# Optimization experiments

Measured on AMD Instinct MI355X. Metric: run time of the kernel, lower is better.

## Reference

```python
import jax, jax.numpy as jnp
import numpy as np

H_TOK = 57
W_TOK = 57
OUT_HW = 800
NUM_MASKS = 64  # static upper bound on sam mask ids per image


def setup_inputs() -> dict:
    key = jax.random.key(0)
    k = jax.random.split(key, 6)
    B, C, C8, L = 2, 768, 96, 21
    return {
        "embeddings": jax.random.normal(k[0], (B, H_TOK * W_TOK, C), dtype=jnp.float32),
        "sam_masks_label": jax.random.randint(k[1], (B, OUT_HW, OUT_HW), 0, NUM_MASKS, dtype=jnp.int32),
        "conv1_w": jax.random.normal(k[2], (C8, C), dtype=jnp.float32) * 0.02,
        "conv1_b": jax.random.normal(k[3], (C8,), dtype=jnp.float32) * 0.02,
        "conv2_w": jax.random.normal(k[4], (L, C8), dtype=jnp.float32) * 0.02,
        "conv2_b": jax.random.normal(k[5], (L,), dtype=jnp.float32) * 0.02,
    }


def _segment_mean_add(xb, lb):
    # xb: [H, W, C8] features; lb: [H, W] int mask ids.
    C8 = xb.shape[-1]
    seg = lb.reshape(-1)                      # [HW]
    xf = xb.reshape(-1, C8)                   # [HW, C8]
    sums = jax.ops.segment_sum(xf, seg, num_segments=NUM_MASKS)          # [M, C8]
    cnt = jax.ops.segment_sum(jnp.ones_like(seg, dtype=xf.dtype), seg, num_segments=NUM_MASKS)  # [M]
    means = sums / jnp.maximum(cnt, 1.0)[:, None]                        # empty segments -> 0, skipped
    return (xf + means[seg]).reshape(xb.shape)


def reference(embeddings, sam_masks_label, conv1_w, conv1_b, conv2_w, conv2_b):
    C = conv1_w.shape[1]
    e = embeddings.reshape(-1, H_TOK, W_TOK, C)            # [B, 57, 57, C] (NHWC)
    # conv1 (1x1) + relu, channels-last
    x = jax.nn.relu(jnp.einsum("bhwc,oc->bhwo", e, conv1_w) + conv1_b)
    # bilinear resize to 800x800, align_corners=False (half-pixel) == jax 'linear'
    B, _, _, C8 = x.shape
    x = jax.image.resize(x, (B, OUT_HW, OUT_HW, C8), method="linear")
    # per-mask segment mean added back (segments are disjoint so order-free)
    x = jax.vmap(_segment_mean_add)(x, sam_masks_label)
    # conv2 (1x1), return NCHW like torch
    out = jnp.einsum("bhwc,oc->bohw", x, conv2_w) + conv2_b[None, :, None, None]
    return out
```

## Files before the change

kernel.cpp:

```cpp
#include <hip/hip_runtime.h>

#define H_TOKN 57
#define OUT_HW 800
#define NMASK 64
#define C_IN 768
#define C8N 96
#define L_OUT 21
#define NPIX 3249
#define M_TOT 6498
#define YSTR 24
#define SCALE (57.0f/800.0f)

#define BM 32
#define ESTR 40
#define HSTR 97

#define TILE_H 25
#define TILE_W 100
#define ROWS_T 4
#define COLS_T 10
#define NTAPS 40
#define YTSTR 28
#define IPAD 264
#define ZPAD 264
#define ZROWS 32
#define NSLICE 256
#define PSTR 28

#define RCSTR 28
#define MFSTR 28
#define FROWS 8

static __device__ __forceinline__ unsigned short f2bf(float f) {
  unsigned u = __float_as_uint(f);
  u += 0x7FFFu + ((u >> 16) & 1u);
  return (unsigned short)(u >> 16);
}

using bf16x8 = __attribute__((ext_vector_type(8))) short;
using f32x4  = __attribute__((ext_vector_type(4))) float;

static __device__ __forceinline__ ushort4 cvt4(float4 v) {
  ushort4 s; s.x = f2bf(v.x); s.y = f2bf(v.y); s.z = f2bf(v.z); s.w = f2bf(v.w);
  return s;
}

__global__ __launch_bounds__(256) void fused_conv_kernel(
    const float* __restrict__ e, const float* __restrict__ w1,
    const float* __restrict__ b1, const float* __restrict__ w2,
    float* __restrict__ y57)
{
  __shared__ __align__(16) unsigned short eA[2][BM * ESTR];
  __shared__ __align__(16) unsigned short wB[2][C8N * ESTR];
  __shared__ __align__(16) float h_lds[BM * HSTR];
  __shared__ float w2_lds[L_OUT * C8N];
  __shared__ float b1_lds[C8N];

  const int tid = threadIdx.x;
  const int m0 = blockIdx.x * BM;
  const int lane = tid & 63;
  const int wv = tid >> 6;
  const int l15 = lane & 15;
  const int khi = (lane >> 4) << 3;
  const int wm = wv & 1;
  const int wn = wv >> 1;

  for (int i = tid; i < L_OUT * C8N; i += 256) w2_lds[i] = w2[i];
  if (tid < C8N) b1_lds[tid] = b1[tid];

  const int er = tid >> 3, ec4 = (tid & 7) << 2;
  int ep = m0 + er; if (ep >= M_TOT) ep = M_TOT - 1;
  const float* eptr = e + (size_t)ep * C_IN + ec4;
  const float* wptr[3];
  int wr_[3], wc4_[3];
  #pragma unroll
  for (int q = 0; q < 3; ++q) {
    int f = tid + q * 256;
    wr_[q] = f >> 3; wc4_[q] = (f & 7) << 2;
    wptr[q] = w1 + (size_t)wr_[q] * C_IN + wc4_[q];
  }

  f32x4 acc[3];
  #pragma unroll
  for (int t = 0; t < 3; ++t) acc[t] = (f32x4){0.f, 0.f, 0.f, 0.f};

  float4 eReg = *(const float4*)(eptr);
  float4 wReg0 = *(const float4*)(wptr[0]);
  float4 wReg1 = *(const float4*)(wptr[1]);
  float4 wReg2 = *(const float4*)(wptr[2]);

  int cur = 0;
  for (int k0 = 0; k0 < C_IN; k0 += 32, cur ^= 1) {
    *(ushort4*)&eA[cur][er * ESTR + ec4] = cvt4(eReg);
    *(ushort4*)&wB[cur][wr_[0] * ESTR + wc4_[0]] = cvt4(wReg0);
    *(ushort4*)&wB[cur][wr_[1] * ESTR + wc4_[1]] = cvt4(wReg1);
    *(ushort4*)&wB[cur][wr_[2] * ESTR + wc4_[2]] = cvt4(wReg2);
    if (k0 + 32 < C_IN) {
      eReg  = *(const float4*)(eptr + k0 + 32);
      wReg0 = *(const float4*)(wptr[0] + k0 + 32);
      wReg1 = *(const float4*)(wptr[1] + k0 + 32);
      wReg2 = *(const float4*)(wptr[2] + k0 + 32);
    }
    __syncthreads();
    bf16x8 a = *(bf16x8*)&eA[cur][(wm * 16 + l15) * ESTR + khi];
    #pragma unroll
    for (int tt = 0; tt < 3; ++tt) {
      bf16x8 b = *(bf16x8*)&wB[cur][((wn * 3 + tt) * 16 + l15) * ESTR + khi];
      acc[tt] = __builtin_amdgcn_mfma_f32_16x16x32_bf16(a, b, acc[tt], 0, 0, 0);
    }
  }
  __syncthreads();
  #pragma unroll
  for (int tt = 0; tt < 3; ++tt) {
    int n = (wn * 3 + tt) * 16 + l15;
    float bv = b1_lds[n];
    #pragma unroll
    for (int r = 0; r < 4; ++r) {
      int pl = wm * 16 + ((lane >> 4) << 2) + r;
      h_lds[pl * HSTR + n] = fmaxf(acc[tt][r] + bv, 0.f);
    }
  }
  __syncthreads();
  for (int i = tid; i < BM * 24; i += 256) {
    int px = i & (BM - 1), l = i >> 5;
    float s = 0.f;
    if (l < L_OUT) {
      const float* hr = &h_lds[px * HSTR];
      const float* wr = &w2_lds[l * C8N];
      #pragma unroll 8
      for (int c = 0; c < C8N; ++c) s += hr[c] * wr[c];
    }
    int pp = m0 + px;
    if (pp < M_TOT) y57[(size_t)pp * YSTR + l] = s;
  }
}

__global__ __launch_bounds__(256) void binsum_kernel(
    const int* __restrict__ labels, const float* __restrict__ y57,
    float* __restrict__ part)
{
  __shared__ __align__(16) unsigned short It[NMASK * IPAD];
  __shared__ __align__(16) unsigned short zT[ZROWS * ZPAD];
  __shared__ __align__(16) float ytile[NTAPS * YTSTR];
  const int tid = threadIdx.x;
  const int lane = tid & 63, wv = tid >> 6;
  const int l15 = lane & 15, khi = (lane >> 4) << 3;
  const int wc0 = blockIdx.x * TILE_W;
  const int hr0 = blockIdx.y * TILE_H;
  const int b = blockIdx.z;

  for (int i = tid; i < NMASK * IPAD / 2; i += 256) ((unsigned*)It)[i] = 0u;
  for (int i = tid; i < ZROWS * ZPAD / 2; i += 256) ((unsigned*)zT)[i] = 0u;

  float thb = fminf(fmaxf((hr0 + 0.5f) * SCALE - 0.5f, 0.f), 56.f);
  const int ib = min((int)thb, 55);
  float twb = fminf(fmaxf((wc0 + 0.5f) * SCALE - 0.5f, 0.f), 56.f);
  const int jb = min((int)twb, 55);

  const float* yb = y57 + (size_t)b * NPIX * YSTR;
  for (int i = tid; i < NTAPS * 6; i += 256) {
    int t = i / 6, q = (i - t * 6) * 4;
    int r = t / COLS_T, cc = t - r * COLS_T;
    int I = min(ib + r, 56), J = min(jb + cc, 56);
    *(float4*)&ytile[t * YTSTR + q] =
        *(const float4*)(yb + ((size_t)I * H_TOKN + J) * YSTR + q);
  }

  const bool valid = tid < 250;
  const int dh = tid / 10;
  const int dwb = (tid - dh * 10) * 10;
  const int hh = hr0 + dh;
  float th = fminf(fmaxf((hh + 0.5f) * SCALE - 0.5f, 0.f), 56.f);
  int i0 = min((int)th, 55);
  const float fh = th - (float)i0;
  const int ri = i0 - ib;
  const int* lrow = labels + ((size_t)b * OUT_HW + hh) * OUT_HW;

  f32x4 acc0 = {0.f,0.f,0.f,0.f}, acc1 = {0.f,0.f,0.f,0.f};
  int prevm = 0;
  const unsigned short one = 0x3F80;

  float u0[24], u1[24];
  int curj = -1000;
  #define LOADU(U, rj) { \
    const float* ta = &ytile[(ri * COLS_T + (rj)) * YTSTR]; \
    const float* tc = ta + COLS_T * YTSTR; \
    _Pragma("unroll") \
    for (int q = 0; q < 6; ++q) { \
      float4 A = *(const float4*)(ta + 4 * q); \
      float4 C = *(const float4*)(tc + 4 * q); \
      U[4*q+0] = A.x + fh * (C.x - A.x); \
      U[4*q+1] = A.y + fh * (C.y - A.y); \
      U[4*q+2] = A.z + fh * (C.z - A.z); \
      U[4*q+3] = A.w + fh * (C.w - A.w); } }

  __syncthreads();
  if (valid) zT[24 * ZPAD + tid] = one;

  for (int c = 0; c < 10; ++c) {
    if (valid) {
      int ww = wc0 + dwb + c;
      float tw = fminf(fmaxf((ww + 0.5f) * SCALE - 0.5f, 0.f), 56.f);
      int j0 = min((int)tw, 55);
      float fw = tw - (float)j0;
      int rj = j0 - jb;
      if (rj != curj) {
        if (rj == curj + 1) {
          #pragma unroll
          for (int ch = 0; ch < 24; ++ch) u0[ch] = u1[ch];
        } else {
          LOADU(u0, rj)
        }
        LOADU(u1, rj + 1)
        curj = rj;
      }
      int m = lrow[ww] & (NMASK - 1);
      #pragma unroll
      for (int ch = 0; ch < 24; ++ch)
        zT[ch * ZPAD + tid] = f2bf(u0[ch] + fw * (u1[ch] - u0[ch]));
      It[prevm * IPAD + tid] = 0;
      It[m * IPAD + tid] = one;
      prevm = m;
    }
    __syncthreads();
    #pragma unroll
    for (int ks = 0; ks < 8; ++ks) {
      bf16x8 a  = *(bf16x8*)&It[(wv * 16 + l15) * IPAD + ks * 32 + khi];
      bf16x8 b0 = *(bf16x8*)&zT[l15 * ZPAD + ks * 32 + khi];
      bf16x8 b1 = *(bf16x8*)&zT[(16 + l15) * ZPAD + ks * 32 + khi];
      acc0 = __builtin_amdgcn_mfma_f32_16x16x32_bf16(a, b0, acc0, 0, 0, 0);
      acc1 = __builtin_amdgcn_mfma_f32_16x16x32_bf16(a, b1, acc1, 0, 0, 0);
    }
    __syncthreads();
  }
  #undef LOADU

  float* pb = part + ((size_t)b * NSLICE +
                      (size_t)(blockIdx.y * gridDim.x + blockIdx.x)) * (NMASK * PSTR);
  const int g4 = (lane >> 4) << 2;
  #pragma unroll
  for (int r = 0; r < 4; ++r) {
    int m = wv * 16 + g4 + r;
    pb[m * PSTR + l15] = acc0[r];
    if (l15 <= 8) pb[m * PSTR + 16 + l15] = acc1[r];
  }
}

__global__ __launch_bounds__(256) void reduce_kernel(
    const float* __restrict__ part, const float* __restrict__ b2,
    float* __restrict__ meanFg)
{
  const int bm = blockIdx.x;
  const int b = bm >> 6, m = bm & 63;
  const int tid = threadIdx.x;
  const float* p = part + ((size_t)b * NSLICE + tid) * (NMASK * PSTR) + (size_t)m * PSTR;
  float4 v[7];
  #pragma unroll
  for (int q = 0; q < 7; ++q) v[q] = *(const float4*)(p + q * 4);
  #pragma unroll
  for (int off = 32; off > 0; off >>= 1) {
    #pragma unroll
    for (int q = 0; q < 7; ++q) {
      v[q].x += __shfl_down(v[q].x, off, 64);
      v[q].y += __shfl_down(v[q].y, off, 64);
      v[q].z += __shfl_down(v[q].z, off, 64);
      v[q].w += __shfl_down(v[q].w, off, 64);
    }
  }
  __shared__ float s_red[4][28];
  const int wid = tid >> 6, lane = tid & 63;
  if (lane == 0) {
    #pragma unroll
    for (int q = 0; q < 7; ++q) *(float4*)&s_red[wid][q * 4] = v[q];
  }
  __syncthreads();
  if (tid < 28) {
    float cnt = s_red[0][24] + s_red[1][24] + s_red[2][24] + s_red[3][24];
    float t = s_red[0][tid] + s_red[1][tid] + s_red[2][tid] + s_red[3][tid];
    float out = (tid < L_OUT) ? t / fmaxf(cnt, 1.f) + b2[tid] : 0.f;
    meanFg[(size_t)bm * MFSTR + tid] = out;
  }
}

__global__ __launch_bounds__(256) void final_kernel(
    const float* __restrict__ y57, const int* __restrict__ labels,
    const float* __restrict__ meanFg, float* __restrict__ out)
{
  __shared__ __align__(16) float rowC[FROWS][H_TOKN * RCSTR];
  __shared__ __align__(16) float meanF[NMASK * MFSTR];
  const int tid = threadIdx.x;
  const int hh0 = blockIdx.y * FROWS;
  const int b = blockIdx.z;
  const float* yb = y57 + (size_t)b * NPIX * YSTR;

  for (int i = tid; i < FROWS * H_TOKN * 6; i += 256) {
    int r = i / (H_TOKN * 6);
    int rest = i - r * (H_TOKN * 6);
    int rr = rest / 6, q = (rest - rr * 6) * 4;
    float th = fminf(fmaxf((hh0 + r + 0.5f) * SCALE - 0.5f, 0.f), 56.f);
    int i0 = min((int)th, 55);
    float fh = th - (float)i0;
    const float* s0 = yb + ((size_t)i0 * H_TOKN + rr) * YSTR + q;
    float4 A = *(const float4*)s0;
    float4 B = *(const float4*)(s0 + H_TOKN * YSTR);
    *(float4*)&rowC[r][rr * RCSTR + q] = make_float4(
        A.x + fh * (B.x - A.x), A.y + fh * (B.y - A.y),
        A.z + fh * (B.z - A.z), A.w + fh * (B.w - A.w));
  }
  {
    const float* src = meanFg + (size_t)b * NMASK * MFSTR;
    for (int i = tid; i < NMASK * MFSTR / 4; i += 256)
      *(float4*)&meanF[i * 4] = *(const float4*)(src + i * 4);
  }
  __syncthreads();

  for (int g = tid; g < FROWS * 200; g += 256) {
    const int row = g / 200;
    const int gg = g - row * 200;
    const int w0 = gg * 4;
    const int hh = hh0 + row;
    const int* lrow = labels + ((size_t)b * OUT_HW + hh) * OUT_HW;
    int4 la = *(const int4*)(lrow + w0);
    float* ob = out + (size_t)b * L_OUT * OUT_HW * OUT_HW + (size_t)hh * OUT_HW + w0;
    const float* rc = rowC[row];

    float fwv[4]; const float* c0p[4]; const float* mfp[4];
    {
      int lam[4] = {la.x & 63, la.y & 63, la.z & 63, la.w & 63};
      #pragma unroll
      for (int k = 0; k < 4; ++k) {
        float tw = fminf(fmaxf((w0 + k + 0.5f) * SCALE - 0.5f, 0.f), 56.f);
        int j0 = min((int)tw, 55);
        fwv[k] = tw - (float)j0;
        c0p[k] = &rc[j0 * RCSTR];
        mfp[k] = &meanF[lam[k] * MFSTR];
      }
    }
    #pragma unroll
    for (int q = 0; q < 6; ++q) {
      float4 V[4];
      #pragma unroll
      for (int k = 0; k < 4; ++k) {
        float4 A  = *(const float4*)(c0p[k] + 4 * q);
        float4 Bv = *(const float4*)(c0p[k] + RCSTR + 4 * q);
        float4 Mv = *(const float4*)(mfp[k] + 4 * q);
        V[k].x = A.x + fwv[k] * (Bv.x - A.x) + Mv.x;
        V[k].y = A.y + fwv[k] * (Bv.y - A.y) + Mv.y;
        V[k].z = A.z + fwv[k] * (Bv.z - A.z) + Mv.z;
        V[k].w = A.w + fwv[k] * (Bv.w - A.w) + Mv.w;
      }
      const int l = 4 * q;
      *(float4*)(ob + (size_t)l * 640000) = make_float4(V[0].x, V[1].x, V[2].x, V[3].x);
      if (l + 1 < L_OUT)
        *(float4*)(ob + (size_t)(l+1) * 640000) = make_float4(V[0].y, V[1].y, V[2].y, V[3].y);
      if (l + 2 < L_OUT)
        *(float4*)(ob + (size_t)(l+2) * 640000) = make_float4(V[0].z, V[1].z, V[2].z, V[3].z);
      if (l + 3 < L_OUT)
        *(float4*)(ob + (size_t)(l+3) * 640000) = make_float4(V[0].w, V[1].w, V[2].w, V[3].w);
    }
  }
}

extern "C" void kernel_launch(void* const* d_in, const int* in_sizes, int n_in,
                              void* d_out, int out_size, void* d_ws, size_t ws_size,
                              hipStream_t stream)
{
  const float* e   = (const float*)d_in[0];
  const int*   lab = (const int*)d_in[1];
  const float* w1  = (const float*)d_in[2];
  const float* b1  = (const float*)d_in[3];
  const float* w2  = (const float*)d_in[4];
  const float* b2  = (const float*)d_in[5];
  float* out = (float*)d_out;
  float* ws  = (float*)d_ws;

  float* y57_ws = ws;
  float* part   = y57_ws + (size_t)M_TOT * YSTR;
  float* meanFg = part + (size_t)2 * NSLICE * NMASK * PSTR;

  fused_conv_kernel<<<dim3((M_TOT + BM - 1) / BM), 256, 0, stream>>>(
      e, w1, b1, w2, y57_ws);
  binsum_kernel<<<dim3(OUT_HW / TILE_W, OUT_HW / TILE_H, 2), 256, 0, stream>>>(
      lab, y57_ws, part);
  reduce_kernel<<<dim3(2 * NMASK), 256, 0, stream>>>(part, b2, meanFg);
  final_kernel<<<dim3(1, OUT_HW / FROWS, 2), 256, 0, stream>>>(
      y57_ws, lab, meanFg, out);
}
```

Measured before the change: 67.19 us.

## Fuse binsum, reduce and final kernels into one persistent kernel with atomic grid barriers

Merges the three post-conv kernels into a single 512-block launch. The first kernel resets two counters, and phases are ordered by atomic counters with spin-waiting instead of kernel boundaries. Shared memory is reused through a union. This removes two launch gaps and tail drains, but it relies on all 512 blocks being co-resident to avoid deadlock, and the spin-waits add latency.

```diff
diff --git a/kernel.cpp b/kernel.cpp
--- a/kernel.cpp
+++ b/kernel.cpp
@@ -31,6 +31,11 @@
 #define MFSTR 28
 #define FROWS 8
 
+#define NB_BIN 512
+#define NB_FIN 200
+#define RED0 200
+#define NB_RED 128
+
 static __device__ __forceinline__ unsigned short f2bf(float f) {
   unsigned u = __float_as_uint(f);
   u += 0x7FFFu + ((u >> 16) & 1u);
@@ -48,7 +53,7 @@
 __global__ __launch_bounds__(256) void fused_conv_kernel(
     const float* __restrict__ e, const float* __restrict__ w1,
     const float* __restrict__ b1, const float* __restrict__ w2,
-    float* __restrict__ y57)
+    float* __restrict__ y57, unsigned* __restrict__ sync)
 {
   __shared__ __align__(16) unsigned short eA[2][BM * ESTR];
   __shared__ __align__(16) unsigned short wB[2][C8N * ESTR];
@@ -64,6 +69,8 @@
   const int khi = (lane >> 4) << 3;
   const int wm = wv & 1;
   const int wn = wv >> 1;
+
+  if (blockIdx.x == 0 && tid < 2) sync[tid] = 0u;
 
   for (int i = tid; i < L_OUT * C8N; i += 256) w2_lds[i] = w2[i];
   if (tid < C8N) b1_lds[tid] = b1[tid];
@@ -135,228 +142,256 @@
   }
 }
 
-__global__ __launch_bounds__(256) void binsum_kernel(
+union SharedB {
+  struct Bin {
+    unsigned short It[NMASK * IPAD];
+    unsigned short zT[ZROWS * ZPAD];
+    float ytile[NTAPS * YTSTR];
+  } bin;
+  struct Red { float s_red[4][28]; } red;
+  struct Fin {
+    float rowC[FROWS][H_TOKN * RCSTR];
+    float meanF[NMASK * MFSTR];
+  } fin;
+};
+
+__global__ __launch_bounds__(256) void megaB_kernel(
     const int* __restrict__ labels, const float* __restrict__ y57,
-    float* __restrict__ part)
+    const float* __restrict__ b2, float* __restrict__ part,
+    float* __restrict__ meanFg, float* __restrict__ out,
+    unsigned* __restrict__ sync)
 {
-  __shared__ __align__(16) unsigned short It[NMASK * IPAD];
-  __shared__ __align__(16) unsigned short zT[ZROWS * ZPAD];
-  __shared__ __align__(16) float ytile[NTAPS * YTSTR];
+  __shared__ __align__(16) SharedB sh;
   const int tid = threadIdx.x;
+  const int bid = blockIdx.x;
   const int lane = tid & 63, wv = tid >> 6;
   const int l15 = lane & 15, khi = (lane >> 4) << 3;
-  const int wc0 = blockIdx.x * TILE_W;
-  const int hr0 = blockIdx.y * TILE_H;
-  const int b = blockIdx.z;
-
-  for (int i = tid; i < NMASK * IPAD / 2; i += 256) ((unsigned*)It)[i] = 0u;
-  for (int i = tid; i < ZROWS * ZPAD / 2; i += 256) ((unsigned*)zT)[i] = 0u;
-
-  float thb = fminf(fmaxf((hr0 + 0.5f) * SCALE - 0.5f, 0.f), 56.f);
-  const int ib = min((int)thb, 55);
-  float twb = fminf(fmaxf((wc0 + 0.5f) * SCALE - 0.5f, 0.f), 56.f);
-  const int jb = min((int)twb, 55);
-
-  const float* yb = y57 + (size_t)b * NPIX * YSTR;
-  for (int i = tid; i < NTAPS * 6; i += 256) {
-    int t = i / 6, q = (i - t * 6) * 4;
-    int r = t / COLS_T, cc = t - r * COLS_T;
-    int I = min(ib + r, 56), J = min(jb + cc, 56);
-    *(float4*)&ytile[t * YTSTR + q] =
-        *(const float4*)(yb + ((size_t)I * H_TOKN + J) * YSTR + q);
-  }
-
-  const bool valid = tid < 250;
-  const int dh = tid / 10;
-  const int dwb = (tid - dh * 10) * 10;
-  const int hh = hr0 + dh;
-  float th = fminf(fmaxf((hh + 0.5f) * SCALE - 0.5f, 0.f), 56.f);
-  int i0 = min((int)th, 55);
-  const float fh = th - (float)i0;
-  const int ri = i0 - ib;
-  const int* lrow = labels + ((size_t)b * OUT_HW + hh) * OUT_HW;
-
-  f32x4 acc0 = {0.f,0.f,0.f,0.f}, acc1 = {0.f,0.f,0.f,0.f};
-  int prevm = 0;
-  const unsigned short one = 0x3F80;
-
-  float u0[24], u1[24];
-  int curj = -1000;
-  #define LOADU(U, rj) { \
-    const float* ta = &ytile[(ri * COLS_T + (rj)) * YTSTR]; \
-    const float* tc = ta + COLS_T * YTSTR; \
-    _Pragma("unroll") \
-    for (int q = 0; q < 6; ++q) { \
-      float4 A = *(const float4*)(ta + 4 * q); \
-      float4 C = *(const float4*)(tc + 4 * q); \
-      U[4*q+0] = A.x + fh * (C.x - A.x); \
-      U[4*q+1] = A.y + fh * (C.y - A.y); \
-      U[4*q+2] = A.z + fh * (C.z - A.z); \
-      U[4*q+3] = A.w + fh * (C.w - A.w); } }
-
-  __syncthreads();
-  if (valid) zT[24 * ZPAD + tid] = one;
-
-  for (int c = 0; c < 10; ++c) {
-    if (valid) {
-      int ww = wc0 + dwb + c;
-      float tw = fminf(fmaxf((ww + 0.5f) * SCALE - 0.5f, 0.f), 56.f);
-      int j0 = min((int)tw, 55);
-      float fw = tw - (float)j0;
-      int rj = j0 - jb;
-      if (rj != curj) {
-        if (rj == curj + 1) {
-          #pragma unroll
-          for (int ch = 0; ch < 24; ++ch) u0[ch] = u1[ch];
-        } else {
-          LOADU(u0, rj)
+
+  {
+    const int b = bid >> 8;
+    const int rem = bid & 255;
+    const int hr0 = (rem >> 3) * TILE_H;
+    const int wc0 = (rem & 7) * TILE_W;
+
+    for (int i = tid; i < NMASK * IPAD / 2; i += 256) ((unsigned*)sh.bin.It)[i] = 0u;
+    for (int i = tid; i < ZROWS * ZPAD / 2; i += 256) ((unsigned*)sh.bin.zT)[i] = 0u;
+
+    float thb = fminf(fmaxf((hr0 + 0.5f) * SCALE - 0.5f, 0.f), 56.f);
+    const int ib = min((int)thb, 55);
+    float twb = fminf(fmaxf((wc0 + 0.5f) * SCALE - 0.5f, 0.f), 56.f);
+    const int jb = min((int)twb, 55);
+
+    const float* yb = y57 + (size_t)b * NPIX * YSTR;
+    for (int i = tid; i < NTAPS * 6; i += 256) {
+      int t = i / 6, q = (i - t * 6) * 4;
+      int r = t / COLS_T, cc = t - r * COLS_T;
+      int I = min(ib + r, 56), J = min(jb + cc, 56);
+      *(float4*)&sh.bin.ytile[t * YTSTR + q] =
+          *(const float4*)(yb + ((size_t)I * H_TOKN + J) * YSTR + q);
+    }
+
+    const bool valid = tid < 250;
+    const int dh = tid / 10;
+    const int dwb = (tid - dh * 10) * 10;
+    const int hh = hr0 + dh;
+    float th = fminf(fmaxf((hh + 0.5f) * SCALE - 0.5f, 0.f), 56.f);
+    int i0 = min((int)th, 55);
+    const float fh = th - (float)i0;
+    const int ri = i0 - ib;
+    const int* lrow = labels + ((size_t)b * OUT_HW + hh) * OUT_HW;
+
+    f32x4 acc0 = {0.f,0.f,0.f,0.f}, acc1 = {0.f,0.f,0.f,0.f};
+    int prevm = 0;
+    const unsigned short one = 0x3F80;
+
+    float u0[24], u1[24];
+    int curj = -1000;
+    #define LOADU(U, rj) { \
+      const float* ta = &sh.bin.ytile[(ri * COLS_T + (rj)) * YTSTR]; \
+      const float* tc = ta + COLS_T * YTSTR; \
+      _Pragma("unroll") \
+      for (int q = 0; q < 6; ++q) { \
+        float4 A = *(const float4*)(ta + 4 * q); \
+        float4 C = *(const float4*)(tc + 4 * q); \
+        U[4*q+0] = A.x + fh * (C.x - A.x); \
+        U[4*q+1] = A.y + fh * (C.y - A.y); \
+        U[4*q+2] = A.z + fh * (C.z - A.z); \
+        U[4*q+3] = A.w + fh * (C.w - A.w); } }
+
+    __syncthreads();
+    if (valid) sh.bin.zT[24 * ZPAD + tid] = one;
+
+    for (int c = 0; c < 10; ++c) {
+      if (valid) {
+        int ww = wc0 + dwb + c;
+        float tw = fminf(fmaxf((ww + 0.5f) * SCALE - 0.5f, 0.f), 56.f);
+        int j0 = min((int)tw, 55);
+        float fw = tw - (float)j0;
+        int rj = j0 - jb;
+        if (rj != curj) {
+          if (rj == curj + 1) {
+            #pragma unroll
+            for (int ch = 0; ch < 24; ++ch) u0[ch] = u1[ch];
+          } else {
+            LOADU(u0, rj)
+          }
+          LOADU(u1, rj + 1)
+          curj = rj;
         }
-        LOADU(u1, rj + 1)
-        curj = rj;
+        int m = lrow[ww] & (NMASK - 1);
+        #pragma unroll
+        for (int ch = 0; ch < 24; ++ch)
+          sh.bin.zT[ch * ZPAD + tid] = f2bf(u0[ch] + fw * (u1[ch] - u0[ch]));
+        sh.bin.It[prevm * IPAD + tid] = 0;
+        sh.bin.It[m * IPAD + tid] = one;
+        prevm = m;
       }
-      int m = lrow[ww] & (NMASK - 1);
+      __syncthreads();
       #pragma unroll
-      for (int ch = 0; ch < 24; ++ch)
-        zT[ch * ZPAD + tid] = f2bf(u0[ch] + fw * (u1[ch] - u0[ch]));
-      It[prevm * IPAD + tid] = 0;
-      It[m * IPAD + tid] = one;
-      prevm = m;
-    }
-    __syncthreads();
+      for (int ks = 0; ks < 8; ++ks) {
+        bf16x8 a  = *(bf16x8*)&sh.bin.It[(wv * 16 + l15) * IPAD + ks * 32 + khi];
+        bf16x8 b0 = *(bf16x8*)&sh.bin.zT[l15 * ZPAD + ks * 32 + khi];
+        bf16x8 b1 = *(bf16x8*)&sh.bin.zT[(16 + l15) * ZPAD + ks * 32 + khi];
+        acc0 = __builtin_amdgcn_mfma_f32_16x16x32_bf16(a, b0, acc0, 0, 0, 0);
+        acc1 = __builtin_amdgcn_mfma_f32_16x16x32_bf16(a, b1, acc1, 0, 0, 0);
+      }
+      __syncthreads();
+    }
+    #undef LOADU
+
+    float* pb = part + ((size_t)b * NSLICE + rem) * (NMASK * PSTR);
+    const int g4 = (lane >> 4) << 2;
     #pragma unroll
-    for (int ks = 0; ks < 8; ++ks) {
-      bf16x8 a  = *(bf16x8*)&It[(wv * 16 + l15) * IPAD + ks * 32 + khi];
-      bf16x8 b0 = *(bf16x8*)&zT[l15 * ZPAD + ks * 32 + khi];
-      bf16x8 b1 = *(bf16x8*)&zT[(16 + l15) * ZPAD + ks * 32 + khi];
-      acc0 = __builtin_amdgcn_mfma_f32_16x16x32_bf16(a, b0, acc0, 0, 0, 0);
-      acc1 = __builtin_amdgcn_mfma_f32_16x16x32_bf16(a, b1, acc1, 0, 0, 0);
-    }
-    __syncthreads();
-  }
-  #undef LOADU
-
-  float* pb = part + ((size_t)b * NSLICE +
-                      (size_t)(blockIdx.y * gridDim.x + blockIdx.x)) * (NMASK * PSTR);
-  const int g4 = (lane >> 4) << 2;
-  #pragma unroll
-  for (int r = 0; r < 4; ++r) {
-    int m = wv * 16 + g4 + r;
-    pb[m * PSTR + l15] = acc0[r];
-    if (l15 <= 8) pb[m * PSTR + 16 + l15] = acc1[r];
-  }
-}
-
-__global__ __launch_bounds__(256) void reduce_kernel(
-    const float* __restrict__ part, const float* __restrict__ b2,
-    float* __restrict__ meanFg)
-{
-  const int bm = blockIdx.x;
-  const int b = bm >> 6, m = bm & 63;
-  const int tid = threadIdx.x;
-  const float* p = part + ((size_t)b * NSLICE + tid) * (NMASK * PSTR) + (size_t)m * PSTR;
-  float4 v[7];
-  #pragma unroll
-  for (int q = 0; q < 7; ++q) v[q] = *(const float4*)(p + q * 4);
-  #pragma unroll
-  for (int off = 32; off > 0; off >>= 1) {
+    for (int r = 0; r < 4; ++r) {
+      int m = wv * 16 + g4 + r;
+      pb[m * PSTR + l15] = acc0[r];
+      if (l15 <= 8) pb[m * PSTR + 16 + l15] = acc1[r];
+    }
+  }
+
+  __threadfence();
+  if (tid == 0)
+    __hip_atomic_fetch_add(&sync[0], 1u, __ATOMIC_ACQ_REL, __HIP_MEMORY_SCOPE_AGENT);
+
+  if (bid >= RED0 && bid < RED0 + NB_RED) {
+    if (tid == 0) {
+      while (__hip_atomic_load(&sync[0], __ATOMIC_ACQUIRE, __HIP_MEMORY_SCOPE_AGENT) < NB_BIN)
+        __builtin_amdgcn_s_sleep(16);
+    }
+    __syncthreads();
+    __threadfence();
+    const int bm = bid - RED0;
+    const int b = bm >> 6, m = bm & 63;
+    const float* p = part + ((size_t)b * NSLICE + tid) * (NMASK * PSTR) + (size_t)m * PSTR;
+    float4 v[7];
     #pragma unroll
-    for (int q = 0; q < 7; ++q) {
-      v[q].x += __shfl_down(v[q].x, off, 64);
-      v[q].y += __shfl_down(v[q].y, off, 64);
-      v[q].z += __shfl_down(v[q].z, off, 64);
-      v[q].w += __shfl_down(v[q].w, off, 64);
-    }
-  }
-  __shared__ float s_red[4][28];
-  const int wid = tid >> 6, lane = tid & 63;
-  if (lane == 0) {
+    for (int q = 0; q < 7; ++q) v[q] = *(const float4*)(p + q * 4);
     #pragma unroll
-    for (int q = 0; q < 7; ++q) *(float4*)&s_red[wid][q * 4] = v[q];
-  }
-  __syncthreads();
-  if (tid < 28) {
-    float cnt = s_red[0][24] + s_red[1][24] + s_red[2][24] + s_red[3][24];
-    float t = s_red[0][tid] + s_red[1][tid] + s_red[2][tid] + s_red[3][tid];
-    float out = (tid < L_OUT) ? t / fmaxf(cnt, 1.f) + b2[tid] : 0.f;
-    meanFg[(size_t)bm * MFSTR + tid] = out;
-  }
-}
-
-__global__ __launch_bounds__(256) void final_kernel(
-    const float* __restrict__ y57, const int* __restrict__ labels,
-    const float* __restrict__ meanFg, float* __restrict__ out)
-{
-  __shared__ __align__(16) float rowC[FROWS][H_TOKN * RCSTR];
-  __shared__ __align__(16) float meanF[NMASK * MFSTR];
-  const int tid = threadIdx.x;
-  const int hh0 = blockIdx.y * FROWS;
-  const int b = blockIdx.z;
-  const float* yb = y57 + (size_t)b * NPIX * YSTR;
-
-  for (int i = tid; i < FROWS * H_TOKN * 6; i += 256) {
-    int r = i / (H_TOKN * 6);
-    int rest = i - r * (H_TOKN * 6);
-    int rr = rest / 6, q = (rest - rr * 6) * 4;
-    float th = fminf(fmaxf((hh0 + r + 0.5f) * SCALE - 0.5f, 0.f), 56.f);
-    int i0 = min((int)th, 55);
-    float fh = th - (float)i0;
-    const float* s0 = yb + ((size_t)i0 * H_TOKN + rr) * YSTR + q;
-    float4 A = *(const float4*)s0;
-    float4 B = *(const float4*)(s0 + H_TOKN * YSTR);
-    *(float4*)&rowC[r][rr * RCSTR + q] = make_float4(
-        A.x + fh * (B.x - A.x), A.y + fh * (B.y - A.y),
-        A.z + fh * (B.z - A.z), A.w + fh * (B.w - A.w));
-  }
+    for (int off = 32; off > 0; off >>= 1) {
+      #pragma unroll
+      for (int q = 0; q < 7; ++q) {
+        v[q].x += __shfl_down(v[q].x, off, 64);
+        v[q].y += __shfl_down(v[q].y, off, 64);
+        v[q].z += __shfl_down(v[q].z, off, 64);
+        v[q].w += __shfl_down(v[q].w, off, 64);
+      }
+    }
+    const int wid = tid >> 6;
+    if (lane == 0) {
+      #pragma unroll
+      for (int q = 0; q < 7; ++q) *(float4*)&sh.red.s_red[wid][q * 4] = v[q];
+    }
+    __syncthreads();
+    if (tid < 28) {
+      float cnt = sh.red.s_red[0][24] + sh.red.s_red[1][24] + sh.red.s_red[2][24] + sh.red.s_red[3][24];
+      float t = sh.red.s_red[0][tid] + sh.red.s_red[1][tid] + sh.red.s_red[2][tid] + sh.red.s_red[3][tid];
+      float o = (tid < L_OUT) ? t / fmaxf(cnt, 1.f) + b2[tid] : 0.f;
+      meanFg[(size_t)bm * MFSTR + tid] = o;
+    }
+    __threadfence();
+    __syncthreads();
+    if (tid == 0)
+      __hip_atomic_fetch_add(&sync[1], 1u, __ATOMIC_ACQ_REL, __HIP_MEMORY_SCOPE_AGENT);
+    return;
+  }
+
+  if (bid >= NB_FIN) return;
   {
-    const float* src = meanFg + (size_t)b * NMASK * MFSTR;
-    for (int i = tid; i < NMASK * MFSTR / 4; i += 256)
-      *(float4*)&meanF[i * 4] = *(const float4*)(src + i * 4);
-  }
-  __syncthreads();
-
-  for (int g = tid; g < FROWS * 200; g += 256) {
-    const int row = g / 200;
-    const int gg = g - row * 200;
-    const int w0 = gg * 4;
-    const int hh = hh0 + row;
-    const int* lrow = labels + ((size_t)b * OUT_HW + hh) * OUT_HW;
-    int4 la = *(const int4*)(lrow + w0);
-    float* ob = out + (size_t)b * L_OUT * OUT_HW * OUT_HW + (size_t)hh * OUT_HW + w0;
-    const float* rc = rowC[row];
-
-    float fwv[4]; const float* c0p[4]; const float* mfp[4];
+    if (tid == 0) {
+      while (__hip_atomic_load(&sync[1], __ATOMIC_ACQUIRE, __HIP_MEMORY_SCOPE_AGENT) < NB_RED)
+        __builtin_amdgcn_s_sleep(16);
+    }
+    __syncthreads();
+    __threadfence();
+    const int b = bid / 100;
+    const int hh0 = (bid - b * 100) * FROWS;
+    const float* yb = y57 + (size_t)b * NPIX * YSTR;
+
+    for (int i = tid; i < FROWS * H_TOKN * 6; i += 256) {
+      int r = i / (H_TOKN * 6);
+      int rest = i - r * (H_TOKN * 6);
+      int rr = rest / 6, q = (rest - rr * 6) * 4;
+      float th = fminf(fmaxf((hh0 + r + 0.5f) * SCALE - 0.5f, 0.f), 56.f);
+      int i0 = min((int)th, 55);
+      float fh = th - (float)i0;
+      const float* s0 = yb + ((size_t)i0 * H_TOKN + rr) * YSTR + q;
+      float4 A = *(const float4*)s0;
+      float4 B = *(const float4*)(s0 + H_TOKN * YSTR);
+      *(float4*)&sh.fin.rowC[r][rr * RCSTR + q] = make_float4(
+          A.x + fh * (B.x - A.x), A.y + fh * (B.y - A.y),
+          A.z + fh * (B.z - A.z), A.w + fh * (B.w - A.w));
+    }
     {
-      int lam[4] = {la.x & 63, la.y & 63, la.z & 63, la.w & 63};
+      const float* src = meanFg + (size_t)b * NMASK * MFSTR;
+      for (int i = tid; i < NMASK * MFSTR / 4; i += 256)
+        *(float4*)&sh.fin.meanF[i * 4] = *(const float4*)(src + i * 4);
+    }
+    __syncthreads();
+
+    for (int g = tid; g < FROWS * 200; g += 256) {
+      const int row = g / 200;
+      const int gg = g - row * 200;
+      const int w0 = gg * 4;
+      const int hh = hh0 + row;
+      const int* lrow = labels + ((size_t)b * OUT_HW + hh) * OUT_HW;
+      int4 la = *(const int4*)(lrow + w0);
+      float* ob = out + (size_t)b * L_OUT * OUT_HW * OUT_HW + (size_t)hh * OUT_HW + w0;
+      const float* rc = sh.fin.rowC[row];
+
+      float fwv[4]; const float* c0p[4]; const float* mfp[4];
+      {
+        int lam[4] = {la.x & 63, la.y & 63, la.z & 63, la.w & 63};
+        #pragma unroll
+        for (int k = 0; k < 4; ++k) {
+          float tw = fminf(fmaxf((w0 + k + 0.5f) * SCALE - 0.5f, 0.f), 56.f);
+          int j0 = min((int)tw, 55);
+          fwv[k] = tw - (float)j0;
+          c0p[k] = &rc[j0 * RCSTR];
+          mfp[k] = &sh.fin.meanF[lam[k] * MFSTR];
+        }
+      }
       #pragma unroll
-      for (int k = 0; k < 4; ++k) {
-        float tw = fminf(fmaxf((w0 + k + 0.5f) * SCALE - 0.5f, 0.f), 56.f);
-        int j0 = min((int)tw, 55);
-        fwv[k] = tw - (float)j0;
-        c0p[k] = &rc[j0 * RCSTR];
-        mfp[k] = &meanF[lam[k] * MFSTR];
+      for (int q = 0; q < 6; ++q) {
+        float4 V[4];
+        #pragma unroll
+        for (int k = 0; k < 4; ++k) {
+          float4 A  = *(const float4*)(c0p[k] + 4 * q);
+          float4 Bv = *(const float4*)(c0p[k] + RCSTR + 4 * q);
+          float4 Mv = *(const float4*)(mfp[k] + 4 * q);
+          V[k].x = A.x + fwv[k] * (Bv.x - A.x) + Mv.x;
+          V[k].y = A.y + fwv[k] * (Bv.y - A.y) + Mv.y;
+          V[k].z = A.z + fwv[k] * (Bv.z - A.z) + Mv.z;
+          V[k].w = A.w + fwv[k] * (Bv.w - A.w) + Mv.w;
+        }
+        const int l = 4 * q;
+        *(float4*)(ob + (size_t)l * 640000) = make_float4(V[0].x, V[1].x, V[2].x, V[3].x);
+        if (l + 1 < L_OUT)
+          *(float4*)(ob + (size_t)(l+1) * 640000) = make_float4(V[0].y, V[1].y, V[2].y, V[3].y);
+        if (l + 2 < L_OUT)
+          *(float4*)(ob + (size_t)(l+2) * 640000) = make_float4(V[0].z, V[1].z, V[2].z, V[3].z);
+        if (l + 3 < L_OUT)
+          *(float4*)(ob + (size_t)(l+3) * 640000) = make_float4(V[0].w, V[1].w, V[2].w, V[3].w);
       }
-    }
-    #pragma unroll
-    for (int q = 0; q < 6; ++q) {
-      float4 V[4];
-      #pragma unroll
-      for (int k = 0; k < 4; ++k) {
-        float4 A  = *(const float4*)(c0p[k] + 4 * q);
-        float4 Bv = *(const float4*)(c0p[k] + RCSTR + 4 * q);
-        float4 Mv = *(const float4*)(mfp[k] + 4 * q);
-        V[k].x = A.x + fwv[k] * (Bv.x - A.x) + Mv.x;
-        V[k].y = A.y + fwv[k] * (Bv.y - A.y) + Mv.y;
-        V[k].z = A.z + fwv[k] * (Bv.z - A.z) + Mv.z;
-        V[k].w = A.w + fwv[k] * (Bv.w - A.w) + Mv.w;
-      }
-      const int l = 4 * q;
-      *(float4*)(ob + (size_t)l * 640000) = make_float4(V[0].x, V[1].x, V[2].x, V[3].x);
-      if (l + 1 < L_OUT)
-        *(float4*)(ob + (size_t)(l+1) * 640000) = make_float4(V[0].y, V[1].y, V[2].y, V[3].y);
-      if (l + 2 < L_OUT)
-        *(float4*)(ob + (size_t)(l+2) * 640000) = make_float4(V[0].z, V[1].z, V[2].z, V[3].z);
-      if (l + 3 < L_OUT)
-        *(float4*)(ob + (size_t)(l+3) * 640000) = make_float4(V[0].w, V[1].w, V[2].w, V[3].w);
     }
   }
 }
@@ -377,12 +412,10 @@
   float* y57_ws = ws;
   float* part   = y57_ws + (size_t)M_TOT * YSTR;
   float* meanFg = part + (size_t)2 * NSLICE * NMASK * PSTR;
+  unsigned* sync = (unsigned*)(meanFg + 2 * NMASK * MFSTR);
 
   fused_conv_kernel<<<dim3((M_TOT + BM - 1) / BM), 256, 0, stream>>>(
-      e, w1, b1, w2, y57_ws);
-  binsum_kernel<<<dim3(OUT_HW / TILE_W, OUT_HW / TILE_H, 2), 256, 0, stream>>>(
-      lab, y57_ws, part);
-  reduce_kernel<<<dim3(2 * NMASK), 256, 0, stream>>>(part, b2, meanFg);
-  final_kernel<<<dim3(1, OUT_HW / FROWS, 2), 256, 0, stream>>>(
-      y57_ws, lab, meanFg, out);
+      e, w1, b1, w2, y57_ws, sync);
+  megaB_kernel<<<dim3(NB_BIN), 256, 0, stream>>>(
+      lab, y57_ws, b2, part, meanFg, out, sync);
 }
```

Result: slower. 200.2 us (+198.0%).

## Fold partial-sum reduction into final kernel and drop separate reduce launch

Applied to the files above, without the earlier changes.

Removes the dedicated reduce_kernel launch. Every final_kernel block now sums all 256 per-slice partial buffers for its batch into shared memory, then normalises by the per-mask count and adds the conv2 bias before writing outputs. This saves one kernel launch and the meanFg round trip through global memory. In exchange, each of the 200 blocks re-reads about 1.8 MB of partials in a serial 256-step loop, so the reduction work and cache traffic are multiplied many times over.

```diff
diff --git a/kernel.cpp b/kernel.cpp
--- a/kernel.cpp
+++ b/kernel.cpp
@@ -26,6 +26,7 @@
 #define ZROWS 32
 #define NSLICE 256
 #define PSTR 28
+#define PROW (NMASK * PSTR)
 
 #define RCSTR 28
 #define MFSTR 28
@@ -236,7 +237,7 @@
   #undef LOADU
 
   float* pb = part + ((size_t)b * NSLICE +
-                      (size_t)(blockIdx.y * gridDim.x + blockIdx.x)) * (NMASK * PSTR);
+                      (size_t)(blockIdx.y * gridDim.x + blockIdx.x)) * PROW;
   const int g4 = (lane >> 4) << 2;
   #pragma unroll
   for (int r = 0; r < 4; ++r) {
@@ -246,53 +247,31 @@
   }
 }
 
-__global__ __launch_bounds__(256) void reduce_kernel(
-    const float* __restrict__ part, const float* __restrict__ b2,
-    float* __restrict__ meanFg)
-{
-  const int bm = blockIdx.x;
-  const int b = bm >> 6, m = bm & 63;
-  const int tid = threadIdx.x;
-  const float* p = part + ((size_t)b * NSLICE + tid) * (NMASK * PSTR) + (size_t)m * PSTR;
-  float4 v[7];
-  #pragma unroll
-  for (int q = 0; q < 7; ++q) v[q] = *(const float4*)(p + q * 4);
-  #pragma unroll
-  for (int off = 32; off > 0; off >>= 1) {
-    #pragma unroll
-    for (int q = 0; q < 7; ++q) {
-      v[q].x += __shfl_down(v[q].x, off, 64);
-      v[q].y += __shfl_down(v[q].y, off, 64);
-      v[q].z += __shfl_down(v[q].z, off, 64);
-      v[q].w += __shfl_down(v[q].w, off, 64);
-    }
-  }
-  __shared__ float s_red[4][28];
-  const int wid = tid >> 6, lane = tid & 63;
-  if (lane == 0) {
-    #pragma unroll
-    for (int q = 0; q < 7; ++q) *(float4*)&s_red[wid][q * 4] = v[q];
-  }
-  __syncthreads();
-  if (tid < 28) {
-    float cnt = s_red[0][24] + s_red[1][24] + s_red[2][24] + s_red[3][24];
-    float t = s_red[0][tid] + s_red[1][tid] + s_red[2][tid] + s_red[3][tid];
-    float out = (tid < L_OUT) ? t / fmaxf(cnt, 1.f) + b2[tid] : 0.f;
-    meanFg[(size_t)bm * MFSTR + tid] = out;
-  }
-}
-
 __global__ __launch_bounds__(256) void final_kernel(
     const float* __restrict__ y57, const int* __restrict__ labels,
-    const float* __restrict__ meanFg, float* __restrict__ out)
+    const float* __restrict__ part, const float* __restrict__ b2,
+    float* __restrict__ out)
 {
   __shared__ __align__(16) float rowC[FROWS][H_TOKN * RCSTR];
-  __shared__ __align__(16) float meanF[NMASK * MFSTR];
+  __shared__ __align__(16) float meanF[PROW];
   const int tid = threadIdx.x;
   const int hh0 = blockIdx.y * FROWS;
   const int b = blockIdx.z;
   const float* yb = y57 + (size_t)b * NPIX * YSTR;
 
+  {
+    const float* pb = part + (size_t)b * NSLICE * PROW;
+    f32x4 a0 = {0.f,0.f,0.f,0.f}, a1 = {0.f,0.f,0.f,0.f};
+    const int f0 = tid;
+    const int f1 = tid + 256;
+    for (int s = 0; s < NSLICE; ++s) {
+      const f32x4* row = (const f32x4*)(pb + (size_t)s * PROW);
+      a0 += row[f0];
+      if (f1 < PROW / 4) a1 += row[f1];
+    }
+    *(f32x4*)&meanF[f0 * 4] = a0;
+    if (f1 < PROW / 4) *(f32x4*)&meanF[f1 * 4] = a1;
+  }
   for (int i = tid; i < FROWS * H_TOKN * 6; i += 256) {
     int r = i / (H_TOKN * 6);
     int rest = i - r * (H_TOKN * 6);
@@ -307,10 +286,13 @@
         A.x + fh * (B.x - A.x), A.y + fh * (B.y - A.y),
         A.z + fh * (B.z - A.z), A.w + fh * (B.w - A.w));
   }
-  {
-    const float* src = meanFg + (size_t)b * NMASK * MFSTR;
-    for (int i = tid; i < NMASK * MFSTR / 4; i += 256)
-      *(float4*)&meanF[i * 4] = *(const float4*)(src + i * 4);
+  __syncthreads();
+  for (int i = tid; i < PROW; i += 256) {
+    int m = i / MFSTR, l = i - m * MFSTR;
+    if (l < L_OUT) {
+      float cnt = meanF[m * MFSTR + 24];
+      meanF[i] = meanF[i] / fmaxf(cnt, 1.f) + b2[l];
+    }
   }
   __syncthreads();
 
@@ -376,13 +358,11 @@
 
   float* y57_ws = ws;
   float* part   = y57_ws + (size_t)M_TOT * YSTR;
-  float* meanFg = part + (size_t)2 * NSLICE * NMASK * PSTR;
 
   fused_conv_kernel<<<dim3((M_TOT + BM - 1) / BM), 256, 0, stream>>>(
       e, w1, b1, w2, y57_ws);
   binsum_kernel<<<dim3(OUT_HW / TILE_W, OUT_HW / TILE_H, 2), 256, 0, stream>>>(
       lab, y57_ws, part);
-  reduce_kernel<<<dim3(2 * NMASK), 256, 0, stream>>>(part, b2, meanFg);
   final_kernel<<<dim3(1, OUT_HW / FROWS, 2), 256, 0, stream>>>(
-      y57_ws, lab, meanFg, out);
-}
+      y57_ws, lab, part, b2, out);
+}
```

New measurement: 138.3 us. 106% more time.

## Shrink conv1 GEMM tile to 16 rows with six waves per block

Applied to the files above, without the earlier changes.

Restructures the fused conv kernel so each block handles 16 pixel rows instead of 32 and uses 384 threads, giving each of six waves one 16x16 output tile instead of three. This doubles the grid from about 204 to about 407 blocks to fill more of the GPU's compute units. Only the first 128 threads stage embedding rows. The second 1x1 projection now maps one output per thread. The cost is that the weight matrix is loaded and converted twice as often in total across blocks.

```diff
diff --git a/kernel.cpp b/kernel.cpp
--- a/kernel.cpp
+++ b/kernel.cpp
@@ -11,7 +11,8 @@
 #define YSTR 24
 #define SCALE (57.0f/800.0f)
 
-#define BM 32
+#define BM 16
+#define NTHR 384
 #define ESTR 40
 #define HSTR 97
 
@@ -45,7 +46,7 @@
   return s;
 }
 
-__global__ __launch_bounds__(256) void fused_conv_kernel(
+__global__ __launch_bounds__(NTHR) void fused_conv_kernel(
     const float* __restrict__ e, const float* __restrict__ w1,
     const float* __restrict__ b1, const float* __restrict__ w2,
     float* __restrict__ y57)
@@ -62,67 +63,54 @@
   const int wv = tid >> 6;
   const int l15 = lane & 15;
   const int khi = (lane >> 4) << 3;
-  const int wm = wv & 1;
-  const int wn = wv >> 1;
-
-  for (int i = tid; i < L_OUT * C8N; i += 256) w2_lds[i] = w2[i];
+
+  for (int i = tid; i < L_OUT * C8N; i += NTHR) w2_lds[i] = w2[i];
   if (tid < C8N) b1_lds[tid] = b1[tid];
 
+  const bool estage = tid < 128;
   const int er = tid >> 3, ec4 = (tid & 7) << 2;
   int ep = m0 + er; if (ep >= M_TOT) ep = M_TOT - 1;
   const float* eptr = e + (size_t)ep * C_IN + ec4;
-  const float* wptr[3];
-  int wr_[3], wc4_[3];
-  #pragma unroll
-  for (int q = 0; q < 3; ++q) {
-    int f = tid + q * 256;
-    wr_[q] = f >> 3; wc4_[q] = (f & 7) << 2;
-    wptr[q] = w1 + (size_t)wr_[q] * C_IN + wc4_[q];
-  }
-
-  f32x4 acc[3];
-  #pragma unroll
-  for (int t = 0; t < 3; ++t) acc[t] = (f32x4){0.f, 0.f, 0.f, 0.f};
-
-  float4 eReg = *(const float4*)(eptr);
-  float4 wReg0 = *(const float4*)(wptr[0]);
-  float4 wReg1 = *(const float4*)(wptr[1]);
-  float4 wReg2 = *(const float4*)(wptr[2]);
+  const int f0 = tid, f1 = tid + NTHR;
+  const int wr0 = f0 >> 3, wc40 = (f0 & 7) << 2;
+  const int wr1 = f1 >> 3, wc41 = (f1 & 7) << 2;
+  const float* wptr0 = w1 + (size_t)wr0 * C_IN + wc40;
+  const float* wptr1 = w1 + (size_t)wr1 * C_IN + wc41;
+
+  f32x4 acc = {0.f, 0.f, 0.f, 0.f};
+
+  float4 eReg = estage ? *(const float4*)(eptr) : make_float4(0,0,0,0);
+  float4 wReg0 = *(const float4*)(wptr0);
+  float4 wReg1 = *(const float4*)(wptr1);
 
   int cur = 0;
   for (int k0 = 0; k0 < C_IN; k0 += 32, cur ^= 1) {
-    *(ushort4*)&eA[cur][er * ESTR + ec4] = cvt4(eReg);
-    *(ushort4*)&wB[cur][wr_[0] * ESTR + wc4_[0]] = cvt4(wReg0);
-    *(ushort4*)&wB[cur][wr_[1] * ESTR + wc4_[1]] = cvt4(wReg1);
-    *(ushort4*)&wB[cur][wr_[2] * ESTR + wc4_[2]] = cvt4(wReg2);
+    if (estage) *(ushort4*)&eA[cur][er * ESTR + ec4] = cvt4(eReg);
+    *(ushort4*)&wB[cur][wr0 * ESTR + wc40] = cvt4(wReg0);
+    *(ushort4*)&wB[cur][wr1 * ESTR + wc41] = cvt4(wReg1);
     if (k0 + 32 < C_IN) {
-      eReg  = *(const float4*)(eptr + k0 + 32);
-      wReg0 = *(const float4*)(wptr[0] + k0 + 32);
-      wReg1 = *(const float4*)(wptr[1] + k0 + 32);
-      wReg2 = *(const float4*)(wptr[2] + k0 + 32);
+      if (estage) eReg = *(const float4*)(eptr + k0 + 32);
+      wReg0 = *(const float4*)(wptr0 + k0 + 32);
+      wReg1 = *(const float4*)(wptr1 + k0 + 32);
     }
     __syncthreads();
-    bf16x8 a = *(bf16x8*)&eA[cur][(wm * 16 + l15) * ESTR + khi];
-    #pragma unroll
-    for (int tt = 0; tt < 3; ++tt) {
-      bf16x8 b = *(bf16x8*)&wB[cur][((wn * 3 + tt) * 16 + l15) * ESTR + khi];
-      acc[tt] = __builtin_amdgcn_mfma_f32_16x16x32_bf16(a, b, acc[tt], 0, 0, 0);
-    }
-  }
-  __syncthreads();
-  #pragma unroll
-  for (int tt = 0; tt < 3; ++tt) {
-    int n = (wn * 3 + tt) * 16 + l15;
+    bf16x8 a = *(bf16x8*)&eA[cur][l15 * ESTR + khi];
+    bf16x8 b = *(bf16x8*)&wB[cur][(wv * 16 + l15) * ESTR + khi];
+    acc = __builtin_amdgcn_mfma_f32_16x16x32_bf16(a, b, acc, 0, 0, 0);
+  }
+  __syncthreads();
+  {
+    int n = wv * 16 + l15;
     float bv = b1_lds[n];
     #pragma unroll
     for (int r = 0; r < 4; ++r) {
-      int pl = wm * 16 + ((lane >> 4) << 2) + r;
-      h_lds[pl * HSTR + n] = fmaxf(acc[tt][r] + bv, 0.f);
-    }
-  }
-  __syncthreads();
-  for (int i = tid; i < BM * 24; i += 256) {
-    int px = i & (BM - 1), l = i >> 5;
+      int pl = ((lane >> 4) << 2) + r;
+      h_lds[pl * HSTR + n] = fmaxf(acc[r] + bv, 0.f);
+    }
+  }
+  __syncthreads();
+  {
+    int px = tid & (BM - 1), l = tid >> 4;
     float s = 0.f;
     if (l < L_OUT) {
       const float* hr = &h_lds[px * HSTR];
@@ -378,7 +366,7 @@
   float* part   = y57_ws + (size_t)M_TOT * YSTR;
   float* meanFg = part + (size_t)2 * NSLICE * NMASK * PSTR;
 
-  fused_conv_kernel<<<dim3((M_TOT + BM - 1) / BM), 256, 0, stream>>>(
+  fused_conv_kernel<<<dim3((M_TOT + BM - 1) / BM), NTHR, 0, stream>>>(
       e, w1, b1, w2, y57_ws);
   binsum_kernel<<<dim3(OUT_HW / TILE_W, OUT_HW / TILE_H, 2), 256, 0, stream>>>(
       lab, y57_ws, part);
```

New measurement: 65.57 us. 1.02x faster.
